# Kernel optimization log

Hardware: AMD Instinct MI355X
Metric: run time of the kernel (lower is better)

The kernel has to match this reference:

```python
import jax, jax.numpy as jnp
import numpy as np

N, HID, H, D = 2048, 1024, 16, 64


def setup_inputs() -> dict:
    key = jax.random.key(0)
    ks = jax.random.split(key, 10)
    s_in = 1.0 / np.sqrt(HID)      # Linear(hidden -> H*D) init scale
    s_o = 1.0 / np.sqrt(H * D)     # Linear(H*D -> D) init scale
    return {
        "x": jax.random.normal(ks[0], (N, HID), jnp.float32),
        "history": jnp.zeros((H, N, N), jnp.float32),
        "Wq_w": jax.random.uniform(ks[1], (H * D, HID), jnp.float32, -s_in, s_in),
        "Wq_b": jax.random.uniform(ks[2], (H * D,), jnp.float32, -s_in, s_in),
        "Wk_w": jax.random.uniform(ks[3], (H * D, HID), jnp.float32, -s_in, s_in),
        "Wk_b": jax.random.uniform(ks[4], (H * D,), jnp.float32, -s_in, s_in),
        "Wv_w": jax.random.uniform(ks[5], (H * D, HID), jnp.float32, -s_in, s_in),
        "Wv_b": jax.random.uniform(ks[6], (H * D,), jnp.float32, -s_in, s_in),
        "Wo_w": jax.random.uniform(ks[7], (D, H * D), jnp.float32, -s_o, s_o),
        "Wo_b": jax.random.uniform(ks[8], (D,), jnp.float32, -s_o, s_o),
        "beta": jnp.float32(0.1),
    }


def reference(x, history, Wq_w, Wq_b, Wk_w, Wk_b, Wv_w, Wv_b, Wo_w, Wo_b, beta):
    n = x.shape[0]
    # QKV projections: [N, H*D] -> [H, N, D]
    q = (x @ Wq_w.T + Wq_b).reshape(n, H, D).transpose(1, 0, 2)
    k = (x @ Wk_w.T + Wk_b).reshape(n, H, D).transpose(1, 0, 2)
    v = (x @ Wv_w.T + Wv_b).reshape(n, H, D).transpose(1, 0, 2)
    scores = jnp.einsum('hnd,hmd->hnm', q, k) / np.sqrt(D).astype(np.float32)
    scores = scores + beta * history  # learned additive history bias
    attn = jax.nn.softmax(scores, axis=-1)  # [H, N, N]
    new_history = history + jax.lax.stop_gradient(attn)  # stateful accumulation (detached)
    out = jnp.einsum('hnm,hmd->hnd', attn, v)  # [H, N, D]
    out = out.transpose(1, 0, 2).reshape(n, H * D)
    out = out @ Wo_w.T + Wo_b  # [N, D]
    # dropout is identity (p=0.0 / eval)
    return (out, attn, new_history)
```

## Files before the change

### kernel.cpp

```cpp
#include <hip/hip_runtime.h>
#include <hip/hip_bf16.h>

#define N_TOK 2048
#define HIDDEN 1024
#define NHEAD 16
#define DHEAD 64

typedef __attribute__((ext_vector_type(8))) short bf16x8;
typedef __attribute__((ext_vector_type(4))) float f32x4;

__device__ inline unsigned short f2bf(float x) {
    __hip_bfloat16 h = __float2bfloat16(x);
    return *reinterpret_cast<unsigned short*>(&h);
}

__device__ inline f32x4 zero4() {
    f32x4 z;
    z[0] = 0.f; z[1] = 0.f; z[2] = 0.f; z[3] = 0.f;
    return z;
}

__global__ void cvt4_kernel(const float* __restrict__ x, const float* __restrict__ wq,
                            const float* __restrict__ wk, const float* __restrict__ wv,
                            unsigned short* __restrict__ dst) {
    int i = blockIdx.x * blockDim.x + threadIdx.x;
    const float* src;
    int off;
    if (i < 524288)       { src = x;  off = i; }
    else if (i < 786432)  { src = wq; off = i - 524288; }
    else if (i < 1048576) { src = wk; off = i - 786432; }
    else                  { src = wv; off = i - 1048576; }
    float4 v = reinterpret_cast<const float4*>(src)[off];
    ushort4 o;
    o.x = f2bf(v.x); o.y = f2bf(v.y); o.z = f2bf(v.z); o.w = f2bf(v.w);
    reinterpret_cast<ushort4*>(dst)[i] = o;
}

__launch_bounds__(256)
__global__ void gemm_qkv(const unsigned short* __restrict__ xb,
                         const unsigned short* __restrict__ wb,
                         const float* __restrict__ bq, const float* __restrict__ bk,
                         const float* __restrict__ bv,
                         unsigned short* __restrict__ qb, unsigned short* __restrict__ kb,
                         unsigned short* __restrict__ vb) {
    __shared__ unsigned short As[2][128 * 64];
    __shared__ unsigned short Bs[2][128 * 64];
    const int tid = threadIdx.x;
    const int lane = tid & 63;
    const int w = tid >> 6;
    const int wr = w >> 1, wc = w & 1;
    const int rb = blockIdx.y * 128;
    const int cb = blockIdx.x * 128;
    const int r0 = tid >> 3, c0 = tid & 7;

    f32x4 acc[4][4];
    for (int i = 0; i < 4; i++)
        for (int j = 0; j < 4; j++) acc[i][j] = zero4();

    uint4 va[4], vb4[4];
#pragma unroll
    for (int i = 0; i < 4; i++) {
        va[i]  = *reinterpret_cast<const uint4*>(xb + (size_t)(rb + r0 + 32 * i) * HIDDEN + c0 * 8);
        vb4[i] = *reinterpret_cast<const uint4*>(wb + (size_t)(cb + r0 + 32 * i) * HIDDEN + c0 * 8);
    }
#pragma unroll
    for (int i = 0; i < 4; i++) {
        int row = r0 + 32 * i;
        *reinterpret_cast<uint4*>(As[0] + row * 64 + ((c0 ^ (row & 7)) << 3)) = va[i];
        *reinterpret_cast<uint4*>(Bs[0] + row * 64 + ((c0 ^ (row & 7)) << 3)) = vb4[i];
    }
    __syncthreads();
    int cur = 0;

    for (int kt = 0; kt < 16; ++kt) {
        if (kt < 15) {
#pragma unroll
            for (int i = 0; i < 4; i++) {
                va[i]  = *reinterpret_cast<const uint4*>(xb + (size_t)(rb + r0 + 32 * i) * HIDDEN + (kt + 1) * 64 + c0 * 8);
                vb4[i] = *reinterpret_cast<const uint4*>(wb + (size_t)(cb + r0 + 32 * i) * HIDDEN + (kt + 1) * 64 + c0 * 8);
            }
        }
#pragma unroll
        for (int kk = 0; kk < 2; kk++) {
            bf16x8 a[4], b[4];
#pragma unroll
            for (int mi = 0; mi < 4; mi++) {
                int row = wr * 64 + mi * 16 + (lane & 15);
                a[mi] = *reinterpret_cast<const bf16x8*>(As[cur] + row * 64 + (((kk * 4 + (lane >> 4)) ^ (row & 7)) << 3));
            }
#pragma unroll
            for (int ni = 0; ni < 4; ni++) {
                int row = wc * 64 + ni * 16 + (lane & 15);
                b[ni] = *reinterpret_cast<const bf16x8*>(Bs[cur] + row * 64 + (((kk * 4 + (lane >> 4)) ^ (row & 7)) << 3));
            }
#pragma unroll
            for (int mi = 0; mi < 4; mi++)
#pragma unroll
                for (int ni = 0; ni < 4; ni++)
                    acc[mi][ni] = __builtin_amdgcn_mfma_f32_16x16x32_bf16(a[mi], b[ni], acc[mi][ni], 0, 0, 0);
        }
        if (kt < 15) {
#pragma unroll
            for (int i = 0; i < 4; i++) {
                int row = r0 + 32 * i;
                *reinterpret_cast<uint4*>(As[cur ^ 1] + row * 64 + ((c0 ^ (row & 7)) << 3)) = va[i];
                *reinterpret_cast<uint4*>(Bs[cur ^ 1] + row * 64 + ((c0 ^ (row & 7)) << 3)) = vb4[i];
            }
        }
        __syncthreads();
        cur ^= 1;
    }

    const int region = blockIdx.x >> 3;
    const float* bias = region == 0 ? bq : (region == 1 ? bk : bv);
    unsigned short* dst = region == 0 ? qb : (region == 1 ? kb : vb);
#pragma unroll
    for (int mi = 0; mi < 4; mi++) {
#pragma unroll
        for (int ni = 0; ni < 4; ni++) {
            int colg = cb + wc * 64 + ni * 16 + (lane & 15);
            int jj = colg & 1023;
            int hh = jj >> 6, d = jj & 63;
            float bval = bias[jj];
#pragma unroll
            for (int r = 0; r < 4; r++) {
                int n = rb + wr * 64 + mi * 16 + ((lane >> 4) << 2) + r;
                dst[((size_t)hh * N_TOK + n) * 64 + d] = f2bf(acc[mi][ni][r] + bval);
            }
        }
    }
}

__global__ void transpose_v(const unsigned short* __restrict__ vb, unsigned short* __restrict__ vt) {
    int t = blockIdx.x * blockDim.x + threadIdx.x;
    int nc = t & 255, d = (t >> 8) & 63, h = t >> 14;
    int n0 = nc * 8;
    unsigned short tmp[8];
#pragma unroll
    for (int j = 0; j < 8; j++)
        tmp[j] = vb[((size_t)h * N_TOK + n0 + j) * 64 + d];
    size_t dsti = (((size_t)(h * 64 + (nc >> 2)) * 64 + d) * 32) + (nc & 3) * 8;
    *reinterpret_cast<uint4*>(vt + dsti) = *reinterpret_cast<uint4*>(tmp);
}

__launch_bounds__(128, 4)
__global__ void attn_fused(const unsigned short* __restrict__ qb,
                           const unsigned short* __restrict__ kb,
                           const unsigned short* __restrict__ vt,
                           const float* __restrict__ hist,
                           const float* __restrict__ beta_p,
                           float* __restrict__ attn_out,
                           float* __restrict__ nh_out,
                           float* __restrict__ hv) {
    __shared__ unsigned short SH[2][4608];
    const int tid = threadIdx.x;
    const int w = tid >> 6;
    const int lane = tid & 63;
    const int g = lane >> 4, q15 = lane & 15;
    const int jr = lane >> 3, jc = lane & 7;
    const int jrv = lane >> 2, jcv = lane & 3;
    const int rb = blockIdx.x, h = blockIdx.y;
    const float beta = beta_p[0];
    const float scale = 0.125f;

    unsigned short* Ksw = SH[w];
    unsigned short* Vsw = SH[w] + 2048;
    unsigned short* Psw = SH[w] + 4096;

    const unsigned short* qsrc = qb + ((size_t)h * N_TOK + rb * 16 + q15) * 64;
    bf16x8 aq0 = *reinterpret_cast<const bf16x8*>(qsrc + 8 * g);
    bf16x8 aq1 = *reinterpret_cast<const bf16x8*>(qsrc + 8 * g + 32);

    const unsigned short* kt0 = kb + (size_t)h * N_TOK * 64 + w * 2048;
    const unsigned short* vt0 = vt + ((size_t)(h * 64 + w)) * 2048;
    const float* hbase = hist + ((size_t)h * N_TOK + rb * 16 + q15) * N_TOK + w * 32 + 4 * g;
    float* abase = attn_out + ((size_t)h * N_TOK + rb * 16 + q15) * N_TOK + w * 32 + 4 * g;
    float* nbase = nh_out + ((size_t)h * N_TOK + rb * 16 + q15) * N_TOK + w * 32 + 4 * g;

    float m = -1e30f, l = 0.0f;
    f32x4 h4[2], h4n[2];

    {
        uint4 kr[4];
#pragma unroll
        for (int i = 0; i < 4; i++)
            kr[i] = *reinterpret_cast<const uint4*>(kt0 + (size_t)(i * 8 + jr) * 64 + jc * 8);
#pragma unroll
        for (int i = 0; i < 4; i++) {
            int row = i * 8 + jr;
            *reinterpret_cast<uint4*>(Ksw + row * 64 + ((jc ^ (row & 7)) << 3)) = kr[i];
        }
#pragma unroll
        for (int nt = 0; nt < 2; nt++) h4[nt] = *reinterpret_cast<const f32x4*>(hbase + nt * 16);
    }

    for (int t = 0; t < 32; t++) {
        uint4 kn[4];
        if (t < 31) {
#pragma unroll
            for (int i = 0; i < 4; i++)
                kn[i] = *reinterpret_cast<const uint4*>(kt0 + (size_t)(t + 1) * 4096 + (size_t)(i * 8 + jr) * 64 + jc * 8);
#pragma unroll
            for (int nt = 0; nt < 2; nt++)
                h4n[nt] = *reinterpret_cast<const f32x4*>(hbase + (t + 1) * 64 + nt * 16);
        }
        f32x4 s_acc[2];
#pragma unroll
        for (int nt = 0; nt < 2; nt++) {
            int krow = nt * 16 + q15;
            bf16x8 kf0 = *reinterpret_cast<const bf16x8*>(Ksw + krow * 64 + ((g ^ (q15 & 7)) << 3));
            bf16x8 kf1 = *reinterpret_cast<const bf16x8*>(Ksw + krow * 64 + (((4 + g) ^ (q15 & 7)) << 3));
            s_acc[nt] = __builtin_amdgcn_mfma_f32_16x16x32_bf16(kf0, aq0, zero4(), 0, 0, 0);
            s_acc[nt] = __builtin_amdgcn_mfma_f32_16x16x32_bf16(kf1, aq1, s_acc[nt], 0, 0, 0);
        }
        float sc[2][4];
#pragma unroll
        for (int nt = 0; nt < 2; nt++)
#pragma unroll
            for (int r = 0; r < 4; r++)
                sc[nt][r] = s_acc[nt][r] * scale + beta * h4[nt][r];

        float tm = sc[0][0];
#pragma unroll
        for (int nt = 0; nt < 2; nt++)
#pragma unroll
            for (int r = 0; r < 4; r++) tm = fmaxf(tm, sc[nt][r]);
        tm = fmaxf(tm, __shfl_xor(tm, 16));
        tm = fmaxf(tm, __shfl_xor(tm, 32));
        float mn = fmaxf(m, tm);
        float ps = 0.0f;
#pragma unroll
        for (int nt = 0; nt < 2; nt++)
#pragma unroll
            for (int r = 0; r < 4; r++) ps += __expf(sc[nt][r] - mn);
        ps += __shfl_xor(ps, 16);
        ps += __shfl_xor(ps, 32);
        l = l * __expf(m - mn) + ps;
        m = mn;

        if (t < 31) {
#pragma unroll
            for (int i = 0; i < 4; i++) {
                int row = i * 8 + jr;
                *reinterpret_cast<uint4*>(Ksw + row * 64 + ((jc ^ (row & 7)) << 3)) = kn[i];
            }
#pragma unroll
            for (int nt = 0; nt < 2; nt++) h4[nt] = h4n[nt];
        }
    }

    float inv_l;
    {
        float* mlbuf = (float*)(SH[0] + 4096);
        if (g == 0) {
            mlbuf[w * 16 + q15] = m;
            mlbuf[32 + w * 16 + q15] = l;
        }
        __syncthreads();
        float m0 = mlbuf[q15], m1 = mlbuf[16 + q15];
        float l0 = mlbuf[32 + q15], l1 = mlbuf[48 + q15];
        float gm = fmaxf(m0, m1);
        float gl = l0 * __expf(m0 - gm) + l1 * __expf(m1 - gm);
        m = gm;
        inv_l = 1.0f / gl;
        __syncthreads();
    }

    f32x4 oacc[4];
#pragma unroll
    for (int di = 0; di < 4; di++) oacc[di] = zero4();

    {
        uint4 vr[4];
#pragma unroll
        for (int i = 0; i < 4; i++)
            vr[i] = *reinterpret_cast<const uint4*>(vt0 + (size_t)31 * 4096 + (size_t)(i * 16 + jrv) * 32 + jcv * 8);
#pragma unroll
        for (int i = 0; i < 4; i++) {
            int row = i * 16 + jrv;
            *reinterpret_cast<uint4*>(Vsw + row * 32 + ((jcv ^ ((row >> 1) & 3)) << 3)) = vr[i];
        }
#pragma unroll
        for (int nt = 0; nt < 2; nt++)
            h4[nt] = *reinterpret_cast<const f32x4*>(hbase + 31 * 64 + nt * 16);
    }

    for (int tt = 0; tt < 32; tt++) {
        const int t = 31 - tt;
        uint4 kn[4], vn[4];
        if (tt < 31) {
#pragma unroll
            for (int i = 0; i < 4; i++) {
                kn[i] = *reinterpret_cast<const uint4*>(kt0 + (size_t)(t - 1) * 4096 + (size_t)(i * 8 + jr) * 64 + jc * 8);
                vn[i] = *reinterpret_cast<const uint4*>(vt0 + (size_t)(t - 1) * 4096 + (size_t)(i * 16 + jrv) * 32 + jcv * 8);
            }
#pragma unroll
            for (int nt = 0; nt < 2; nt++)
                h4n[nt] = *reinterpret_cast<const f32x4*>(hbase + (t - 1) * 64 + nt * 16);
        }

        f32x4 s_acc[2];
#pragma unroll
        for (int nt = 0; nt < 2; nt++) {
            int krow = nt * 16 + q15;
            bf16x8 kf0 = *reinterpret_cast<const bf16x8*>(Ksw + krow * 64 + ((g ^ (q15 & 7)) << 3));
            bf16x8 kf1 = *reinterpret_cast<const bf16x8*>(Ksw + krow * 64 + (((4 + g) ^ (q15 & 7)) << 3));
            s_acc[nt] = __builtin_amdgcn_mfma_f32_16x16x32_bf16(kf0, aq0, zero4(), 0, 0, 0);
            s_acc[nt] = __builtin_amdgcn_mfma_f32_16x16x32_bf16(kf1, aq1, s_acc[nt], 0, 0, 0);
        }

#pragma unroll
        for (int nt = 0; nt < 2; nt++) {
            float a0 = __expf(s_acc[nt][0] * scale + beta * h4[nt][0] - m) * inv_l;
            float a1 = __expf(s_acc[nt][1] * scale + beta * h4[nt][1] - m) * inv_l;
            float a2 = __expf(s_acc[nt][2] * scale + beta * h4[nt][2] - m) * inv_l;
            float a3 = __expf(s_acc[nt][3] * scale + beta * h4[nt][3] - m) * inv_l;
            f32x4 av, nv;
            av[0] = a0; av[1] = a1; av[2] = a2; av[3] = a3;
            nv[0] = a0 + h4[nt][0]; nv[1] = a1 + h4[nt][1];
            nv[2] = a2 + h4[nt][2]; nv[3] = a3 + h4[nt][3];
            __builtin_nontemporal_store(av, reinterpret_cast<f32x4*>(abase + t * 64 + nt * 16));
            __builtin_nontemporal_store(nv, reinterpret_cast<f32x4*>(nbase + t * 64 + nt * 16));
            ushort4 p;
            p.x = f2bf(a0); p.y = f2bf(a1); p.z = f2bf(a2); p.w = f2bf(a3);
            *reinterpret_cast<ushort4*>(Psw + q15 * 32 + (((4 * nt + g) ^ (q15 & 6)) << 2)) = p;
        }

        {
            bf16x8 pa = *reinterpret_cast<const bf16x8*>(Psw + q15 * 32 + (((2 * g) ^ (q15 & 6)) << 2));
#pragma unroll
            for (int di = 0; di < 4; di++) {
                int vrow = di * 16 + q15;
                bf16x8 vf = *reinterpret_cast<const bf16x8*>(Vsw + vrow * 32 + ((g ^ ((q15 >> 1) & 3)) << 3));
                oacc[di] = __builtin_amdgcn_mfma_f32_16x16x32_bf16(pa, vf, oacc[di], 0, 0, 0);
            }
        }

        if (tt < 31) {
#pragma unroll
            for (int i = 0; i < 4; i++) {
                int row = i * 8 + jr;
                *reinterpret_cast<uint4*>(Ksw + row * 64 + ((jc ^ (row & 7)) << 3)) = kn[i];
            }
#pragma unroll
            for (int i = 0; i < 4; i++) {
                int row = i * 16 + jrv;
                *reinterpret_cast<uint4*>(Vsw + row * 32 + ((jcv ^ ((row >> 1) & 3)) << 3)) = vn[i];
            }
#pragma unroll
            for (int nt = 0; nt < 2; nt++) h4[nt] = h4n[nt];
        }
    }

    {
        float* vbuf = (float*)(SH[1] + 2048);
        if (w == 1) {
#pragma unroll
            for (int di = 0; di < 4; di++)
#pragma unroll
                for (int r = 0; r < 4; r++)
                    vbuf[(4 * g + r) * 64 + di * 16 + q15] = oacc[di][r];
        }
        __syncthreads();
        if (w == 0) {
#pragma unroll
            for (int di = 0; di < 4; di++) {
#pragma unroll
                for (int r = 0; r < 4; r++) {
                    int rl = 4 * g + r;
                    int d = di * 16 + q15;
                    hv[((size_t)h * N_TOK + rb * 16 + rl) * 64 + d] =
                        oacc[di][r] + vbuf[rl * 64 + d];
                }
            }
        }
    }
}

__launch_bounds__(256)
__global__ void out_proj(const float* __restrict__ hv, const float* __restrict__ Wo,
                         const float* __restrict__ bo, float* __restrict__ out) {
    __shared__ float wos[64][129];
    const int tid = threadIdx.x;
    const int dd = tid & 63;
    const int w = tid >> 6;
    const int n0 = blockIdx.x * 16;
    float acc[4] = {0.f, 0.f, 0.f, 0.f};
    for (int kc = 0; kc < 1024; kc += 128) {
        __syncthreads();
#pragma unroll
        for (int i = 0; i < 32; i++) {
            int e = tid + 256 * i;
            int r = e >> 7, j = e & 127;
            wos[r][j] = Wo[(size_t)r * 1024 + kc + j];
        }
        __syncthreads();
#pragma unroll 4
        for (int k = 0; k < 128; k++) {
            float wv = wos[dd][k];
            int jg = kc + k;
            const float* hb = hv + ((size_t)(jg >> 6) * N_TOK) * 64 + (jg & 63);
#pragma unroll
            for (int q = 0; q < 4; q++) {
                acc[q] += hb[(size_t)(n0 + w + 4 * q) * 64] * wv;
            }
        }
    }
#pragma unroll
    for (int q = 0; q < 4; q++)
        out[(size_t)(n0 + w + 4 * q) * 64 + dd] = acc[q] + bo[dd];
}

extern "C" void kernel_launch(void* const* d_in, const int* in_sizes, int n_in,
                              void* d_out, int out_size, void* d_ws, size_t ws_size,
                              hipStream_t stream) {
    const float* x    = (const float*)d_in[0];
    const float* hist = (const float*)d_in[1];
    const float* Wq_w = (const float*)d_in[2];
    const float* Wq_b = (const float*)d_in[3];
    const float* Wk_w = (const float*)d_in[4];
    const float* Wk_b = (const float*)d_in[5];
    const float* Wv_w = (const float*)d_in[6];
    const float* Wv_b = (const float*)d_in[7];
    const float* Wo_w = (const float*)d_in[8];
    const float* Wo_b = (const float*)d_in[9];
    const float* beta = (const float*)d_in[10];

    float* out = (float*)d_out;
    float* attn_out = out + 131072;
    float* nh_out = attn_out + (size_t)NHEAD * N_TOK * N_TOK;

    unsigned short* xb  = (unsigned short*)d_ws;
    unsigned short* wb  = xb + (size_t)N_TOK * HIDDEN;
    unsigned short* qb  = wb + (size_t)3 * HIDDEN * HIDDEN;
    unsigned short* kb  = qb + (size_t)N_TOK * HIDDEN;
    unsigned short* vb  = kb + (size_t)N_TOK * HIDDEN;
    unsigned short* vt  = vb + (size_t)N_TOK * HIDDEN;
    float* hvb = (float*)(vt + (size_t)N_TOK * HIDDEN);

    cvt4_kernel<<<5120, 256, 0, stream>>>(x, Wq_w, Wk_w, Wv_w, xb);
    gemm_qkv<<<dim3(24, 16), 256, 0, stream>>>(xb, wb, Wq_b, Wk_b, Wv_b, qb, kb, vb);
    transpose_v<<<1024, 256, 0, stream>>>(vb, vt);
    attn_fused<<<dim3(128, 16), 128, 0, stream>>>(qb, kb, vt, hist, beta,
                                                  attn_out, nh_out, hvb);
    out_proj<<<128, 256, 0, stream>>>(hvb, Wo_w, Wo_b, out);
}
```

Before: 557.7 us.

## Fuse V transpose into QKV GEMM epilogue and pin attention load waits

The QKV GEMM epilogue now writes V straight into the transposed tiled layout the attention kernel expects, which removes the separate transpose_v kernel and its extra round trip through global memory. In the attention kernel's two passes, sched_barrier markers and explicit s_waitcnt vmcnt instructions pin where prefetched K/V/history loads are waited on before the LDS writes. The goal is to keep the compiler from hoisting or sinking those waits, so the loads overlap with compute. In exchange, the V epilogue stores are scattered 2-byte writes with poor coalescing, and the hand-chosen vmcnt values depend on load ordering and could be fragile.

```diff
diff --git a/kernel.cpp b/kernel.cpp
--- a/kernel.cpp
+++ b/kernel.cpp
@@ -8,6 +8,8 @@
 
 typedef __attribute__((ext_vector_type(8))) short bf16x8;
 typedef __attribute__((ext_vector_type(4))) float f32x4;
+
+#define SB() __builtin_amdgcn_sched_barrier(0)
 
 __device__ inline unsigned short f2bf(float x) {
     __hip_bfloat16 h = __float2bfloat16(x);
@@ -42,7 +44,7 @@
                          const float* __restrict__ bq, const float* __restrict__ bk,
                          const float* __restrict__ bv,
                          unsigned short* __restrict__ qb, unsigned short* __restrict__ kb,
-                         unsigned short* __restrict__ vb) {
+                         unsigned short* __restrict__ vt) {
     __shared__ unsigned short As[2][128 * 64];
     __shared__ unsigned short Bs[2][128 * 64];
     const int tid = threadIdx.x;
@@ -113,7 +115,7 @@
 
     const int region = blockIdx.x >> 3;
     const float* bias = region == 0 ? bq : (region == 1 ? bk : bv);
-    unsigned short* dst = region == 0 ? qb : (region == 1 ? kb : vb);
+    unsigned short* dst = region == 0 ? qb : kb;
 #pragma unroll
     for (int mi = 0; mi < 4; mi++) {
 #pragma unroll
@@ -125,22 +127,14 @@
 #pragma unroll
             for (int r = 0; r < 4; r++) {
                 int n = rb + wr * 64 + mi * 16 + ((lane >> 4) << 2) + r;
-                dst[((size_t)hh * N_TOK + n) * 64 + d] = f2bf(acc[mi][ni][r] + bval);
-            }
-        }
-    }
-}
-
-__global__ void transpose_v(const unsigned short* __restrict__ vb, unsigned short* __restrict__ vt) {
-    int t = blockIdx.x * blockDim.x + threadIdx.x;
-    int nc = t & 255, d = (t >> 8) & 63, h = t >> 14;
-    int n0 = nc * 8;
-    unsigned short tmp[8];
-#pragma unroll
-    for (int j = 0; j < 8; j++)
-        tmp[j] = vb[((size_t)h * N_TOK + n0 + j) * 64 + d];
-    size_t dsti = (((size_t)(h * 64 + (nc >> 2)) * 64 + d) * 32) + (nc & 3) * 8;
-    *reinterpret_cast<uint4*>(vt + dsti) = *reinterpret_cast<uint4*>(tmp);
+                unsigned short val = f2bf(acc[mi][ni][r] + bval);
+                if (region < 2)
+                    dst[((size_t)hh * N_TOK + n) * 64 + d] = val;
+                else
+                    vt[(((size_t)(hh * 64 + (n >> 5)) * 64 + d) * 32) + (n & 31)] = val;
+            }
+        }
+    }
 }
 
 __launch_bounds__(128, 4)
@@ -203,6 +197,7 @@
 #pragma unroll
             for (int nt = 0; nt < 2; nt++)
                 h4n[nt] = *reinterpret_cast<const f32x4*>(hbase + (t + 1) * 64 + nt * 16);
+            SB();
         }
         f32x4 s_acc[2];
 #pragma unroll
@@ -239,6 +234,9 @@
         m = mn;
 
         if (t < 31) {
+            SB();
+            asm volatile("s_waitcnt vmcnt(0)" ::: "memory");
+            SB();
 #pragma unroll
             for (int i = 0; i < 4; i++) {
                 int row = i * 8 + jr;
@@ -297,6 +295,7 @@
 #pragma unroll
             for (int nt = 0; nt < 2; nt++)
                 h4n[nt] = *reinterpret_cast<const f32x4*>(hbase + (t - 1) * 64 + nt * 16);
+            SB();
         }
 
         f32x4 s_acc[2];
@@ -337,6 +336,9 @@
         }
 
         if (tt < 31) {
+            SB();
+            asm volatile("s_waitcnt vmcnt(4)" ::: "memory");
+            SB();
 #pragma unroll
             for (int i = 0; i < 4; i++) {
                 int row = i * 8 + jr;
@@ -434,13 +436,11 @@
     unsigned short* wb  = xb + (size_t)N_TOK * HIDDEN;
     unsigned short* qb  = wb + (size_t)3 * HIDDEN * HIDDEN;
     unsigned short* kb  = qb + (size_t)N_TOK * HIDDEN;
-    unsigned short* vb  = kb + (size_t)N_TOK * HIDDEN;
-    unsigned short* vt  = vb + (size_t)N_TOK * HIDDEN;
+    unsigned short* vt  = kb + (size_t)N_TOK * HIDDEN;
     float* hvb = (float*)(vt + (size_t)N_TOK * HIDDEN);
 
     cvt4_kernel<<<5120, 256, 0, stream>>>(x, Wq_w, Wk_w, Wv_w, xb);
-    gemm_qkv<<<dim3(24, 16), 256, 0, stream>>>(xb, wb, Wq_b, Wk_b, Wv_b, qb, kb, vb);
-    transpose_v<<<1024, 256, 0, stream>>>(vb, vt);
+    gemm_qkv<<<dim3(24, 16), 256, 0, stream>>>(xb, wb, Wq_b, Wk_b, Wv_b, qb, kb, vt);
     attn_fused<<<dim3(128, 16), 128, 0, stream>>>(qb, kb, vt, hist, beta,
                                                   attn_out, nh_out, hvb);
     out_proj<<<128, 256, 0, stream>>>(hvb, Wo_w, Wo_b, out);
```

Measured after the change: 558.9 us. No clear change (+0.2%).
